# Optimization experiments

Hardware: AMD Instinct MI355X
Metric: run time of the kernel (lower is better)

The kernel has to match this reference:

```python
import jax, jax.numpy as jnp
import numpy as np
import math

B, S, H = 1, 2048, 2048
NH, NKV, HD = 32, 8, 64
GROUPS = NH // NKV
WINDOW = 128
ROPE_THETA = 150000.0
FACTOR = 32.0
ORIG_MAX = 4096.0
BETA_FAST = 32.0
BETA_SLOW = 1.0
SCALE = 1.0 / math.sqrt(HD)


def yarn_rope(q, k, position_ids):
    # q: [B,S,NH,HD], k: [B,S,NKV,HD]
    dim_half = HD // 2
    inv_freq = 1.0 / ROPE_THETA ** (jnp.arange(0, dim_half, 2, dtype=jnp.float32) / dim_half)
    wavelengths = 2.0 * jnp.pi / inv_freq
    ratio = ORIG_MAX / wavelengths
    alpha = jnp.clip((FACTOR * ratio - BETA_FAST) / (BETA_SLOW - BETA_FAST), 0.0, 1.0)
    inv_freq_scaled = inv_freq / FACTOR ** alpha
    freqs = position_ids[:, :, None].astype(jnp.float32) * inv_freq_scaled[None, None, :]
    freqs = jnp.repeat(freqs, 2, axis=-1)  # [B,S,dim_half]
    cos = jnp.cos(freqs)[:, :, None, :]
    sin = jnp.sin(freqs)[:, :, None, :]

    def rotate_half(x):
        # Faithful to source: x already has last dim == dim_half, so x2 is empty
        # and rotate_half(x) == x. Kept literal for exactness.
        x1 = x[..., :dim_half]
        x2 = x[..., dim_half:]
        return jnp.concatenate([-x2, x1], axis=-1)

    q_rot = q[..., :dim_half]
    k_rot = k[..., :dim_half]
    q_rot = q_rot * cos + rotate_half(q_rot) * sin
    k_rot = k_rot * cos + rotate_half(k_rot) * sin
    q = jnp.concatenate([q_rot, q[..., dim_half:]], axis=-1)
    k = jnp.concatenate([k_rot, k[..., dim_half:]], axis=-1)
    return q, k


def setup_inputs() -> dict:
    key = jax.random.key(0)
    ks = jax.random.split(key, 5)
    std = 0.02
    hidden_states = jax.random.normal(ks[0], (B, S, H), dtype=jnp.float32)
    position_ids = jnp.broadcast_to(jnp.arange(S, dtype=jnp.int32)[None, :], (B, S))
    Wq = jax.random.normal(ks[1], (H, NH * HD), dtype=jnp.float32) * std
    Wk = jax.random.normal(ks[2], (H, NKV * HD), dtype=jnp.float32) * std
    Wv = jax.random.normal(ks[3], (H, NKV * HD), dtype=jnp.float32) * std
    Wo = jax.random.normal(ks[4], (NH * HD, H), dtype=jnp.float32) * std
    return {"hidden_states": hidden_states, "position_ids": position_ids,
            "Wq": Wq, "Wk": Wk, "Wv": Wv, "Wo": Wo}


def reference(hidden_states, position_ids, Wq, Wk, Wv, Wo):
    q = (hidden_states @ Wq).reshape(B, S, NH, HD)
    k = (hidden_states @ Wk).reshape(B, S, NKV, HD)
    v = (hidden_states @ Wv).reshape(B, S, NKV, HD)
    q, k = yarn_rope(q, k, position_ids)
    # GQA: repeat kv heads to match query heads
    k = jnp.repeat(k, GROUPS, axis=2)  # [B,S,NH,HD]
    v = jnp.repeat(v, GROUPS, axis=2)
    # scores: [B,NH,S,S]
    scores = jnp.einsum('bqhd,bkhd->bhqk', q, k) * SCALE
    row = jnp.arange(S)[:, None]
    col = jnp.arange(S)[None, :]
    mask = ((jnp.abs(row - col) <= WINDOW) & (row >= col)).astype(jnp.float32)
    scores = scores + (1.0 - mask)[None, None, :, :] * -1e9
    attn = jax.nn.softmax(scores, axis=-1)
    out = jnp.einsum('bhqk,bkhd->bqhd', attn, v).reshape(B, S, NH * HD)
    return out @ Wo
```

## Files before the change

kernel.cpp:

```cpp
#include <hip/hip_runtime.h>

typedef unsigned short u16;
typedef short short8 __attribute__((ext_vector_type(8)));
typedef float f32x4 __attribute__((ext_vector_type(4)));

#define SLEN 2048
#define QKV_LD 3072
#define KOFF 2048
#define VOFF 2560

__device__ __forceinline__ u16 f2b(float f){
  unsigned u = __float_as_uint(f);
  u = u + 0x7FFFu + ((u >> 16) & 1u);
  return (u16)(u >> 16);
}
__device__ __forceinline__ float b2f(u16 v){
  unsigned u = ((unsigned)v) << 16;
  return __uint_as_float(u);
}

__device__ __forceinline__ void gload16(const u16* g, u16* l){
  __builtin_amdgcn_global_load_lds((const __attribute__((address_space(1))) void*)g,
                                   (__attribute__((address_space(3))) void*)l, 16, 0, 0);
}

__global__ __launch_bounds__(256) void k_prep(const float* __restrict__ hidden, u16* __restrict__ hb,
                                              const int* __restrict__ pos, float* __restrict__ g,
                                              const float* __restrict__ Wq, const float* __restrict__ Wk,
                                              const float* __restrict__ Wv, const float* __restrict__ Wo,
                                              u16* __restrict__ Wcat, u16* __restrict__ Wot){
  __shared__ float tile[64][68];
  int b = blockIdx.x, t = threadIdx.x;
  if (b < 4096){
    int i = b * 256 + t;
    float4 v = ((const float4*)hidden)[i];
    ushort4 o;
    o.x = f2b(v.x); o.y = f2b(v.y); o.z = f2b(v.z); o.w = f2b(v.w);
    ((ushort4*)hb)[i] = o;
    return;
  }
  if (b < 4224){
    int idx = (b - 4096) * 256 + t;
    int s = idx >> 4, i = idx & 15;
    float inv = 1.0f / powf(150000.0f, (float)i / 16.0f);
    float wl = 6.283185307179586f / inv;
    float ratio = 4096.0f / wl;
    float alpha = (32.0f * ratio - 32.0f) / (1.0f - 32.0f);
    alpha = fminf(fmaxf(alpha, 0.0f), 1.0f);
    float invs = inv / powf(32.0f, alpha);
    float th = (float)pos[s] * invs;
    double tt = (double)th;
    g[idx] = (float)(cos(tt) + sin(tt));
    return;
  }
  b -= 4224;
  const float* W; u16* D; int Nw, rowoff;
  if (b < 1024)      { W = Wq; D = Wcat; Nw = 2048; rowoff = 0; }
  else if (b < 1280) { W = Wk; D = Wcat; Nw = 512;  rowoff = 2048; b -= 1024; }
  else if (b < 1536) { W = Wv; D = Wcat; Nw = 512;  rowoff = 2560; b -= 1280; }
  else               { W = Wo; D = Wot;  Nw = 2048; rowoff = 0;    b -= 1536; }
  const int kt = b & 31, nt = b >> 5;
  const int k0 = kt * 64, n0 = nt * 64;
  #pragma unroll
  for (int i = 0; i < 4; ++i){
    int slot = i * 256 + t;
    int r = slot >> 4, c4 = (slot & 15) * 4;
    float4 v = *(const float4*)&W[(size_t)(k0 + r) * Nw + n0 + c4];
    tile[r][c4] = v.x; tile[r][c4+1] = v.y; tile[r][c4+2] = v.z; tile[r][c4+3] = v.w;
  }
  __syncthreads();
  #pragma unroll
  for (int i = 0; i < 4; ++i){
    int slot = i * 256 + t;
    int nl = slot >> 4, k4 = (slot & 15) * 4;
    ushort4 o;
    o.x = f2b(tile[k4][nl]);   o.y = f2b(tile[k4+1][nl]);
    o.z = f2b(tile[k4+2][nl]); o.w = f2b(tile[k4+3][nl]);
    *(ushort4*)&D[(size_t)(rowoff + n0 + nl) * 2048 + k0 + k4] = o;
  }
}

template<int OUTF32, int ROPE, int BM, int BN, int MINW>
__global__ __launch_bounds__(256, MINW) void k_gemm(const u16* __restrict__ A, const u16* __restrict__ Bt,
                                                    void* __restrict__ C, const float* __restrict__ g,
                                                    int M, int N, int K){
  constexpr int AG = BM / 32;
  constexpr int BG = BN / 32;
  constexpr int ASZ = BM * 64;
  constexpr int BSZ = BN * 64;
  constexpr int MR = BM / 32;
  constexpr int NR = BN / 32;
  __shared__ __align__(16) u16 Smem[2 * (ASZ + BSZ)];
  const int tid = threadIdx.x;
  const int lane = tid & 63;
  const int w = tid >> 6;
  const int wr = (w >> 1) * (BM / 2);
  const int wc = (w & 1) * (BN / 2);

  const int nbx = M / BM;
  const int nb  = nbx * (N / BN);
  const int q8  = nb >> 3;
  const int bo  = blockIdx.x;
  const int id2 = (bo & 7) * q8 + (bo >> 3);
  const int m0 = (id2 % nbx) * BM;
  const int n0 = (id2 / nbx) * BN;

  const int rl = lane >> 3;
  const int sc = ((lane & 7) ^ rl) << 3;
  const u16* Ag[AG]; const u16* Bg[BG];
  int Ad[AG], Bd[BG];
  #pragma unroll
  for (int i = 0; i < AG; ++i){
    int row0 = w * (AG * 8) + i * 8;
    Ag[i] = A + (size_t)(m0 + row0 + rl) * K + sc;
    Ad[i] = row0 * 64;
  }
  #pragma unroll
  for (int i = 0; i < BG; ++i){
    int row0 = w * (BG * 8) + i * 8;
    Bg[i] = Bt + (size_t)(n0 + row0 + rl) * K + sc;
    Bd[i] = 2 * ASZ + row0 * 64;
  }

  const int fr = lane & 15;
  const int g4 = lane >> 4;

  f32x4 acc[MR][NR] = {};

  auto stage = [&](int buf, int k0){
    #pragma unroll
    for (int i = 0; i < AG; ++i) gload16(Ag[i] + k0, Smem + Ad[i] + buf * ASZ);
    #pragma unroll
    for (int i = 0; i < BG; ++i) gload16(Bg[i] + k0, Smem + Bd[i] + buf * BSZ);
  };

  stage(0, 0);
  int buf = 0;
  const int nt = K >> 6;
  for (int kt = 0; kt < nt; ++kt){
    if (kt + 1 < nt){
      stage(buf ^ 1, (kt + 1) << 6);
      if constexpr (AG + BG == 6)      asm volatile("s_waitcnt vmcnt(6)" ::: "memory");
      else if constexpr (AG + BG == 7) asm volatile("s_waitcnt vmcnt(7)" ::: "memory");
      else                             asm volatile("s_waitcnt vmcnt(8)" ::: "memory");
    } else {
      asm volatile("s_waitcnt vmcnt(0)" ::: "memory");
    }
    __builtin_amdgcn_s_barrier();
    __builtin_amdgcn_sched_barrier(0);
    {
      const u16* Asb = Smem + buf * ASZ;
      const u16* Bsb = Smem + 2 * ASZ + buf * BSZ;
      #pragma unroll
      for (int kk = 0; kk < 2; ++kk){
        const int sw = (((kk * 4 + g4)) ^ (fr & 7)) << 3;
        short8 af[MR], bf[NR];
        #pragma unroll
        for (int m = 0; m < MR; ++m)
          af[m] = *(const short8*)&Asb[(wr + m * 16 + fr) * 64 + sw];
        #pragma unroll
        for (int j = 0; j < NR; ++j)
          bf[j] = *(const short8*)&Bsb[(wc + j * 16 + fr) * 64 + sw];
        #pragma unroll
        for (int m = 0; m < MR; ++m)
          #pragma unroll
          for (int j = 0; j < NR; ++j)
            acc[m][j] = __builtin_amdgcn_mfma_f32_16x16x32_bf16(af[m], bf[j], acc[m][j], 0, 0, 0);
      }
    }
    __builtin_amdgcn_sched_barrier(0);
    __builtin_amdgcn_s_barrier();
    buf ^= 1;
  }

  const int r4 = g4 * 4;
  #pragma unroll
  for (int m = 0; m < MR; ++m)
    #pragma unroll
    for (int j = 0; j < NR; ++j)
      #pragma unroll
      for (int v = 0; v < 4; ++v){
        size_t row = (size_t)(m0 + wr + m * 16 + r4 + v);
        size_t col = (size_t)(n0 + wc + j * 16 + fr);
        float x = acc[m][j][v];
        if (OUTF32){
          ((float*)C)[row * N + col] = x;
        } else {
          if (ROPE){
            int c = (int)col;
            int cj = c & 63;
            if (c < 2560 && cj < 32) x *= g[row * 16 + (cj >> 1)];
            if (c < 2048) x *= 0.125f;
          }
          ((u16*)C)[row * N + col] = f2b(x);
        }
      }
}

__global__ __launch_bounds__(256, 3) void k_attn(const u16* __restrict__ qkv, u16* __restrict__ aout){
  __shared__ __align__(16) u16 Vt[64 * 200];
  __shared__ __align__(16) u16 P[64 * 200];
  const int tid = threadIdx.x;
  const int lane = tid & 63;
  const int w = tid >> 6;
  const int id = blockIdx.x;
  const int o = (id & 7) * 128 + (id >> 3);
  const int h = o >> 5;
  const int q0 = (o & 31) * 64;
  const int kvh = h >> 2;
  const int kv0 = q0 - 128;
  {
    const u16* Vg = qkv + VOFF + kvh * 64;
    #pragma unroll
    for (int i = 0; i < 6; ++i){
      int slot = i * 256 + tid;
      int kk = slot >> 3, d8 = (slot & 7) * 8;
      int ks = kv0 + kk; if (ks < 0) ks = 0;
      int ck = kk ^ ((d8 >> 4) << 3);
      short8 v = *(const short8*)(Vg + (size_t)ks * QKV_LD + d8);
      #pragma unroll
      for (int e = 0; e < 8; ++e) Vt[(d8 + e) * 200 + ck] = (u16)v[e];
    }
  }
  __syncthreads();

  const int fr = lane & 15;
  const int kc8 = (lane >> 4) * 8;
  const int r4 = (lane >> 4) * 4;
  const int nw0 = w & ~1;
  const int c0 = nw0 * 16;
  const u16* Qg = qkv + h * 64;
  const u16* Kg = qkv + KOFF + kvh * 64;
  const int kbase = kv0;

  short8 qa[2];
  {
    int qrow = q0 + w * 16 + fr;
    qa[0] = *(const short8*)(Qg + (size_t)qrow * QKV_LD + kc8);
    qa[1] = *(const short8*)(Qg + (size_t)qrow * QKV_LD + 32 + kc8);
  }

  f32x4 sc[10];
  #pragma unroll
  for (int n = 0; n < 10; ++n){
    int kr = kbase + (nw0 + n) * 16 + fr;
    int krc = kr < 0 ? 0 : kr;
    short8 kb0 = *(const short8*)(Kg + (size_t)krc * QKV_LD + kc8);
    short8 kb1 = *(const short8*)(Kg + (size_t)krc * QKV_LD + 32 + kc8);
    f32x4 z = {0.f, 0.f, 0.f, 0.f};
    z = __builtin_amdgcn_mfma_f32_16x16x32_bf16(qa[0], kb0, z, 0, 0, 0);
    z = __builtin_amdgcn_mfma_f32_16x16x32_bf16(qa[1], kb1, z, 0, 0, 0);
    sc[n] = z;
  }

  float inv_l[4];
  #pragma unroll
  for (int j = 0; j < 4; ++j){
    int q = q0 + w * 16 + r4 + j;
    float mx = -3.0e38f;
    #pragma unroll
    for (int n = 0; n < 10; ++n){
      int key = kbase + (nw0 + n) * 16 + fr;
      bool valid = (key >= 0) && (key <= q) && (key >= q - 128);
      float s = valid ? sc[n][j] : -1.0e30f;
      sc[n][j] = s;
      mx = fmaxf(mx, s);
    }
    mx = fmaxf(mx, __shfl_xor(mx, 1));
    mx = fmaxf(mx, __shfl_xor(mx, 2));
    mx = fmaxf(mx, __shfl_xor(mx, 4));
    mx = fmaxf(mx, __shfl_xor(mx, 8));
    float sum = 0.f;
    #pragma unroll
    for (int n = 0; n < 10; ++n){
      float pp = exp2f((sc[n][j] - mx) * 1.4426950408889634f);
      sc[n][j] = pp;
      sum += pp;
    }
    sum += __shfl_xor(sum, 1);
    sum += __shfl_xor(sum, 2);
    sum += __shfl_xor(sum, 4);
    sum += __shfl_xor(sum, 8);
    inv_l[j] = 1.0f / sum;
  }

  #pragma unroll
  for (int n = 0; n < 10; ++n)
    #pragma unroll
    for (int j = 0; j < 4; ++j)
      P[(w * 16 + r4 + j) * 200 + n * 16 + fr] = f2b(sc[n][j]);

  asm volatile("s_waitcnt lgkmcnt(0)" ::: "memory");

  f32x4 ov[4] = {};
  #pragma unroll
  for (int kc = 0; kc < 5; ++kc){
    short8 pa = *(const short8*)&P[(w * 16 + fr) * 200 + kc * 32 + kc8];
    #pragma unroll
    for (int f = 0; f < 4; ++f){
      short8 vb = *(const short8*)&Vt[(f * 16 + fr) * 200 + c0 + kc * 32 + (kc8 ^ (f << 3))];
      ov[f] = __builtin_amdgcn_mfma_f32_16x16x32_bf16(pa, vb, ov[f], 0, 0, 0);
    }
  }

  #pragma unroll
  for (int f = 0; f < 4; ++f)
    #pragma unroll
    for (int j = 0; j < 4; ++j){
      int q = q0 + w * 16 + r4 + j;
      int col = h * 64 + f * 16 + fr;
      aout[(size_t)q * 2048 + col] = f2b(ov[f][j] * inv_l[j]);
    }
}

extern "C" void kernel_launch(void* const* d_in, const int* in_sizes, int n_in,
                              void* d_out, int out_size, void* d_ws, size_t ws_size,
                              hipStream_t stream) {
  const float* hidden = (const float*)d_in[0];
  const int*   pos    = (const int*)d_in[1];
  const float* Wq     = (const float*)d_in[2];
  const float* Wk     = (const float*)d_in[3];
  const float* Wv     = (const float*)d_in[4];
  const float* Wo     = (const float*)d_in[5];
  float* out = (float*)d_out;
  char* ws = (char*)d_ws;

  u16*  hb   = (u16*)(ws);
  u16*  Wcat = (u16*)(ws + ((size_t)8 << 20));
  u16*  Wot  = (u16*)(ws + ((size_t)20 << 20));
  u16*  QKV  = (u16*)(ws + ((size_t)28 << 20));
  float* gtab = (float*)(ws + ((size_t)40 << 20));
  u16*  aout = hb;

  k_prep<<<6784, 256, 0, stream>>>(hidden, hb, pos, gtab, Wq, Wk, Wv, Wo, Wcat, Wot);
  k_gemm<0,1,128,96,2><<<512, 256, 0, stream>>>(hb, Wcat, QKV, gtab, 2048, 3072, 2048);
  k_attn<<<1024, 256, 0, stream>>>(QKV, aout);
  k_gemm<1,0,64,128,3><<<512, 256, 0, stream>>>(aout, Wot, out, nullptr, 2048, 2048, 2048);
}
```

Measured before the change: 101.8 us.

## Write V transposed from QKV GEMM epilogue and read it directly in attention

The QKV projection epilogue now writes the V columns in transposed [d][seq] layout into a separate global buffer instead of into the QKV matrix. The attention kernel drops its LDS staging and transposition of V and loads V operand fragments straight from global memory. P gets a smaller per-wave LDS buffer, and the occupancy hint is raised from 3 to 4. The cost is that V^T stores from the GEMM epilogue are strided by 2048 elements, which coalesce poorly, and V fragment reads now go through global memory and cache.

After: 106.2 us. 1.04x slower.

```diff
diff --git a/kernel.cpp b/kernel.cpp
--- a/kernel.cpp
+++ b/kernel.cpp
@@ -7,7 +7,6 @@
 #define SLEN 2048
 #define QKV_LD 3072
 #define KOFF 2048
-#define VOFF 2560
 
 __device__ __forceinline__ u16 f2b(float f){
   unsigned u = __float_as_uint(f);
@@ -83,6 +82,7 @@
 template<int OUTF32, int ROPE, int BM, int BN, int MINW>
 __global__ __launch_bounds__(256, MINW) void k_gemm(const u16* __restrict__ A, const u16* __restrict__ Bt,
                                                     void* __restrict__ C, const float* __restrict__ g,
+                                                    u16* __restrict__ Vtg,
                                                     int M, int N, int K){
   constexpr int AG = BM / 32;
   constexpr int BG = BN / 32;
@@ -185,53 +185,43 @@
         float x = acc[m][j][v];
         if (OUTF32){
           ((float*)C)[row * N + col] = x;
+        } else if (ROPE){
+          int c = (int)col;
+          int cj = c & 63;
+          if (c < 2560 && cj < 32) x *= g[row * 16 + (cj >> 1)];
+          if (c < 2048) x *= 0.125f;
+          if (c >= 2560) Vtg[(size_t)(c - 2560) * 2048 + row] = f2b(x);
+          else           ((u16*)C)[row * N + col] = f2b(x);
         } else {
-          if (ROPE){
-            int c = (int)col;
-            int cj = c & 63;
-            if (c < 2560 && cj < 32) x *= g[row * 16 + (cj >> 1)];
-            if (c < 2048) x *= 0.125f;
-          }
           ((u16*)C)[row * N + col] = f2b(x);
         }
       }
 }
 
-__global__ __launch_bounds__(256, 3) void k_attn(const u16* __restrict__ qkv, u16* __restrict__ aout){
-  __shared__ __align__(16) u16 Vt[64 * 200];
-  __shared__ __align__(16) u16 P[64 * 200];
+#define PST 168
+__global__ __launch_bounds__(256, 4) void k_attn(const u16* __restrict__ qkv,
+                                                 const u16* __restrict__ Vtg,
+                                                 u16* __restrict__ aout){
+  __shared__ __align__(16) u16 P[4 * 16 * PST];
   const int tid = threadIdx.x;
   const int lane = tid & 63;
   const int w = tid >> 6;
   const int id = blockIdx.x;
-  const int o = (id & 7) * 128 + (id >> 3);
-  const int h = o >> 5;
-  const int q0 = (o & 31) * 64;
+  const int id2 = (id & 7) * 128 + (id >> 3);
+  const int h = id2 >> 5;
+  const int q0 = (id2 & 31) * 64;
   const int kvh = h >> 2;
-  const int kv0 = q0 - 128;
-  {
-    const u16* Vg = qkv + VOFF + kvh * 64;
-    #pragma unroll
-    for (int i = 0; i < 6; ++i){
-      int slot = i * 256 + tid;
-      int kk = slot >> 3, d8 = (slot & 7) * 8;
-      int ks = kv0 + kk; if (ks < 0) ks = 0;
-      int ck = kk ^ ((d8 >> 4) << 3);
-      short8 v = *(const short8*)(Vg + (size_t)ks * QKV_LD + d8);
-      #pragma unroll
-      for (int e = 0; e < 8; ++e) Vt[(d8 + e) * 200 + ck] = (u16)v[e];
-    }
-  }
-  __syncthreads();
+  const int kbase = q0 - 128;
 
   const int fr = lane & 15;
   const int kc8 = (lane >> 4) * 8;
   const int r4 = (lane >> 4) * 4;
   const int nw0 = w & ~1;
   const int c0 = nw0 * 16;
+  u16* Pw = P + w * 16 * PST;
   const u16* Qg = qkv + h * 64;
   const u16* Kg = qkv + KOFF + kvh * 64;
-  const int kbase = kv0;
+  const u16* Vg = Vtg + (size_t)(kvh * 64) * 2048;
 
   short8 qa[2];
   {
@@ -288,17 +278,19 @@
   for (int n = 0; n < 10; ++n)
     #pragma unroll
     for (int j = 0; j < 4; ++j)
-      P[(w * 16 + r4 + j) * 200 + n * 16 + fr] = f2b(sc[n][j]);
+      Pw[(r4 + j) * PST + n * 16 + fr] = f2b(sc[n][j]);
 
   asm volatile("s_waitcnt lgkmcnt(0)" ::: "memory");
 
   f32x4 ov[4] = {};
   #pragma unroll
   for (int kc = 0; kc < 5; ++kc){
-    short8 pa = *(const short8*)&P[(w * 16 + fr) * 200 + kc * 32 + kc8];
+    short8 pa = *(const short8*)&Pw[fr * PST + kc * 32 + kc8];
+    int kb = kbase + c0 + kc * 32 + kc8;
+    if (kb < 0) kb = 0;
     #pragma unroll
     for (int f = 0; f < 4; ++f){
-      short8 vb = *(const short8*)&Vt[(f * 16 + fr) * 200 + c0 + kc * 32 + (kc8 ^ (f << 3))];
+      short8 vb = *(const short8*)(Vg + (size_t)(f * 16 + fr) * 2048 + kb);
       ov[f] = __builtin_amdgcn_mfma_f32_16x16x32_bf16(pa, vb, ov[f], 0, 0, 0);
     }
   }
@@ -330,10 +322,11 @@
   u16*  Wot  = (u16*)(ws + ((size_t)20 << 20));
   u16*  QKV  = (u16*)(ws + ((size_t)28 << 20));
   float* gtab = (float*)(ws + ((size_t)40 << 20));
+  u16*  Vtg  = (u16*)(ws + ((size_t)41 << 20));
   u16*  aout = hb;
 
   k_prep<<<6784, 256, 0, stream>>>(hidden, hb, pos, gtab, Wq, Wk, Wv, Wo, Wcat, Wot);
-  k_gemm<0,1,128,96,2><<<512, 256, 0, stream>>>(hb, Wcat, QKV, gtab, 2048, 3072, 2048);
-  k_attn<<<1024, 256, 0, stream>>>(QKV, aout);
-  k_gemm<1,0,64,128,3><<<512, 256, 0, stream>>>(aout, Wot, out, nullptr, 2048, 2048, 2048);
-}
+  k_gemm<0,1,128,96,2><<<512, 256, 0, stream>>>(hb, Wcat, QKV, gtab, Vtg, 2048, 3072, 2048);
+  k_attn<<<1024, 256, 0, stream>>>(QKV, Vtg, aout);
+  k_gemm<1,0,64,128,3><<<512, 256, 0, stream>>>(aout, Wot, out, nullptr, nullptr, 2048, 2048, 2048);
+}
```
